# Kernel optimization log

Hardware: AMD Instinct MI355X
Metric: run time of the kernel (lower is better)

The kernel has to match this reference:

```python
import jax, jax.numpy as jnp
import numpy as np

EPS = 1e-5
N_NODES = 100000


def setup_inputs() -> dict:
    key = jax.random.key(0)
    ks = jax.random.split(key, 24)
    N, F = N_NODES, 64
    E = 1600000
    inp = {
        "x": jax.random.normal(ks[0], (N, F), dtype=jnp.float32),
        "edge_index": jax.random.randint(ks[1], (2, E), 0, N, dtype=jnp.int64),
    }
    dims = [(F, 32), (32, 64), (64, 128), (128, 1)]
    for i, (din, dout) in enumerate(dims, start=1):
        kw, kb = jax.random.split(ks[1 + i], 2)
        scale = 1.0 / np.sqrt(din)
        inp[f"W{i}"] = jax.random.uniform(kw, (din, dout), jnp.float32, -scale, scale)
        inp[f"b{i}"] = jax.random.uniform(kb, (dout,), jnp.float32, -scale, scale)
    for i, d in enumerate([32, 64, 128], start=1):
        kg, kbe, km, kv = jax.random.split(ks[8 + i], 4)
        inp[f"g{i}"] = 1.0 + 0.1 * jax.random.normal(kg, (d,), jnp.float32)
        inp[f"be{i}"] = 0.1 * jax.random.normal(kbe, (d,), jnp.float32)
        inp[f"rm{i}"] = 0.1 * jax.random.normal(km, (d,), jnp.float32)
        inp[f"rv{i}"] = 0.5 + jax.random.uniform(kv, (d,), jnp.float32)
    return inp


def _gcn_conv(x, src, dst, norm, W, b, n):
    # GCNConv: linear transform then D^-1/2 A_hat D^-1/2 aggregation (self-loops in src/dst)
    xw = x @ W  # [N, dout]
    msg = xw[src] * norm[:, None]  # [E+N, dout] gather
    return jax.ops.segment_sum(msg, dst, num_segments=n) + b


def _bn_eval(x, g, be, rm, rv):
    return (x - rm) * jax.lax.rsqrt(rv + EPS) * g + be


def reference(x, edge_index, W1, b1, W2, b2, W3, b3, W4, b4,
              g1, be1, rm1, rv1, g2, be2, rm2, rv2, g3, be3, rm3, rv3):
    n = x.shape[0]
    loop = jnp.arange(n, dtype=edge_index.dtype)
    src = jnp.concatenate([edge_index[0], loop])
    dst = jnp.concatenate([edge_index[1], loop])
    deg = jax.ops.segment_sum(jnp.ones_like(dst, dtype=x.dtype), dst, num_segments=n)
    dinv = jnp.where(deg > 0, jax.lax.rsqrt(deg), 0.0)
    norm = dinv[src] * dinv[dst]  # shared across layers

    h = _gcn_conv(x, src, dst, norm, W1, b1, n)
    h = jax.nn.elu(_bn_eval(h, g1, be1, rm1, rv1))
    h = _gcn_conv(h, src, dst, norm, W2, b2, n)
    h = jax.nn.elu(_bn_eval(h, g2, be2, rm2, rv2))
    h = _gcn_conv(h, src, dst, norm, W3, b3, n)
    h = jax.nn.elu(_bn_eval(h, g3, be3, rm3, rv3))
    h = _gcn_conv(h, src, dst, norm, W4, b4, n)
    return jax.nn.sigmoid(jax.nn.elu(h))
```

## Files before the change

kernel.cpp:

```cpp
#include <hip/hip_runtime.h>
#include <hip/hip_fp16.h>

#define EPSF 1e-5f
#define BKT_SHIFT 9
#define BKT_NODES 512
#define TILE_E 4096

__device__ __forceinline__ float elu_f(float x) { return x > 0.f ? x : expm1f(x); }

__device__ __forceinline__ float4 h4_to_f4(uint2 u) {
    __half2 a = *reinterpret_cast<const __half2*>(&u.x);
    __half2 b = *reinterpret_cast<const __half2*>(&u.y);
    float2 fa = __half22float2(a);
    float2 fb = __half22float2(b);
    return make_float4(fa.x, fa.y, fb.x, fb.y);
}
__device__ __forceinline__ uint2 f4_to_h4(float4 v) {
    __half2 a = __floats2half2_rn(v.x, v.y);
    __half2 b = __floats2half2_rn(v.z, v.w);
    uint2 u;
    u.x = *reinterpret_cast<unsigned*>(&a);
    u.y = *reinterpret_cast<unsigned*>(&b);
    return u;
}


__global__ __launch_bounds__(256) void k_zero(int* p, int n) {
    int i = blockIdx.x * 256 + threadIdx.x;
    if (i < n) p[i] = 0;
}

__global__ __launch_bounds__(256) void k_bhist(const int* __restrict__ dst, int* __restrict__ bkt_cnt, int E) {
    __shared__ int h[256];
    int t = threadIdx.x;
    h[t] = 0;
    __syncthreads();
    for (long e = (long)blockIdx.x * 256 + t; e < E; e += (long)gridDim.x * 256)
        atomicAdd(&h[dst[e] >> BKT_SHIFT], 1);
    __syncthreads();
    if (h[t]) atomicAdd(&bkt_cnt[t], h[t]);
}

__global__ __launch_bounds__(256) void k_bscan(const int* __restrict__ bkt_cnt, int* __restrict__ bbase,
                                               int* __restrict__ cursor) {
    __shared__ int sh[256];
    int t = threadIdx.x;
    int v = bkt_cnt[t];
    sh[t] = v;
    __syncthreads();
    for (int off = 1; off < 256; off <<= 1) {
        int add = (t >= off) ? sh[t - off] : 0;
        __syncthreads();
        sh[t] += add;
        __syncthreads();
    }
    int ex = sh[t] - v;
    bbase[t] = ex;
    cursor[t] = ex;
}

__global__ __launch_bounds__(256) void k_bpart(const int* __restrict__ src, const int* __restrict__ dst,
                                               int* __restrict__ cursor, int2* __restrict__ csr_tmp, int E) {
    __shared__ int hcnt[256];
    __shared__ int gbase[256];
    int t = threadIdx.x;
    long tile0 = (long)blockIdx.x * TILE_E;
    hcnt[t] = 0;
    __syncthreads();
    int d[16], s[16], rk[16];
    #pragma unroll
    for (int j = 0; j < 16; ++j) {
        long e = tile0 + j * 256 + t;
        if (e < E) {
            d[j] = dst[e];
            s[j] = src[e];
            rk[j] = atomicAdd(&hcnt[d[j] >> BKT_SHIFT], 1);
        }
    }
    __syncthreads();
    int c = hcnt[t];
    if (c) gbase[t] = atomicAdd(&cursor[t], c);
    __syncthreads();
    #pragma unroll
    for (int j = 0; j < 16; ++j) {
        long e = tile0 + j * 256 + t;
        if (e < E) {
            int2 q;
            q.x = d[j];
            q.y = s[j];
            csr_tmp[gbase[d[j] >> BKT_SHIFT] + rk[j]] = q;
        }
    }
}

__global__ __launch_bounds__(256) void k_bfine(const int2* __restrict__ csr_tmp, const int* __restrict__ bbase,
                                               const int* __restrict__ bkt_cnt, int* __restrict__ cnt,
                                               int* __restrict__ base, float* __restrict__ dinv,
                                               int* __restrict__ csr_s, int N) {
    __shared__ int cnt5[BKT_NODES];
    __shared__ int off5[BKT_NODES];
    __shared__ int sh[256];
    int b = blockIdx.x;
    int t = threadIdx.x;
    int d0 = b << BKT_SHIFT;
    int bb = bbase[b];
    int bc = bkt_cnt[b];
    cnt5[t] = 0;
    cnt5[t + 256] = 0;
    __syncthreads();
    for (int k = t; k < bc; k += 256) atomicAdd(&cnt5[csr_tmp[bb + k].x - d0], 1);
    __syncthreads();
    int v0 = cnt5[2 * t], v1 = cnt5[2 * t + 1];
    int p = v0 + v1;
    sh[t] = p;
    __syncthreads();
    for (int off = 1; off < 256; off <<= 1) {
        int add = (t >= off) ? sh[t - off] : 0;
        __syncthreads();
        sh[t] += add;
        __syncthreads();
    }
    int pre = sh[t] - p;
    off5[2 * t] = pre;
    off5[2 * t + 1] = pre + v0;
    #pragma unroll
    for (int j = 0; j < 2; ++j) {
        int idx = 2 * t + j;
        int i = d0 + idx;
        if (i < N) {
            int c = cnt5[idx];
            base[i] = bb + off5[idx];
            cnt[i] = c;
            dinv[i] = rsqrtf((float)(c + 1));
        }
    }
    __syncthreads();
    for (int k = t; k < bc; k += 256) {
        int2 e = csr_tmp[bb + k];
        int pos = bb + atomicAdd(&off5[e.x - d0], 1);
        csr_s[pos] = e.y;
    }
}

template<int F, bool L1EPI, bool HIN, bool HOUT>
__global__ __launch_bounds__(256) void k_gather(const int* __restrict__ base, const int* __restrict__ cnt,
                                                const int* __restrict__ csr_s,
                                                const float* __restrict__ dinv, const void* __restrict__ xin,
                                                const float* __restrict__ b, const float* __restrict__ g,
                                                const float* __restrict__ be, const float* __restrict__ rm,
                                                const float* __restrict__ rv, void* __restrict__ out, int n) {
    constexpr int C = F / 4;
    constexpr int NPB = 256 / C;
    int lane = threadIdx.x % C;
    int nl = threadIdx.x / C;
    int i = blockIdx.x * NPB + nl;
    if (i >= n) return;
    int k = base[i];
    int kend = k + cnt[i];
    float di = dinv[i];
    const float4* XF = reinterpret_cast<const float4*>(xin);
    const uint2*  XH = reinterpret_cast<const uint2*>(xin);
    float4 z = {0.f, 0.f, 0.f, 0.f};
    float4 a0 = z, a1 = z, a2 = z, a3 = z;
    for (; k + 3 < kend; k += 4) {
        int s0 = csr_s[k], s1 = csr_s[k + 1], s2 = csr_s[k + 2], s3 = csr_s[k + 3];
        float4 x0 = HIN ? h4_to_f4(XH[(long)s0 * C + lane]) : XF[(long)s0 * C + lane];
        float4 x1 = HIN ? h4_to_f4(XH[(long)s1 * C + lane]) : XF[(long)s1 * C + lane];
        float4 x2 = HIN ? h4_to_f4(XH[(long)s2 * C + lane]) : XF[(long)s2 * C + lane];
        float4 x3 = HIN ? h4_to_f4(XH[(long)s3 * C + lane]) : XF[(long)s3 * C + lane];
        a0.x += x0.x; a0.y += x0.y; a0.z += x0.z; a0.w += x0.w;
        a1.x += x1.x; a1.y += x1.y; a1.z += x1.z; a1.w += x1.w;
        a2.x += x2.x; a2.y += x2.y; a2.z += x2.z; a2.w += x2.w;
        a3.x += x3.x; a3.y += x3.y; a3.z += x3.z; a3.w += x3.w;
    }
    for (; k < kend; ++k) {
        int s0 = csr_s[k];
        float4 xa = HIN ? h4_to_f4(XH[(long)s0 * C + lane]) : XF[(long)s0 * C + lane];
        a0.x += xa.x; a0.y += xa.y; a0.z += xa.z; a0.w += xa.w;
    }
    float4 xs = HIN ? h4_to_f4(XH[(long)i * C + lane]) : XF[(long)i * C + lane];
    float4 o;
    o.x = di * (a0.x + a1.x + a2.x + a3.x + xs.x);
    o.y = di * (a0.y + a1.y + a2.y + a3.y + xs.y);
    o.z = di * (a0.z + a1.z + a2.z + a3.z + xs.z);
    o.w = di * (a0.w + a1.w + a2.w + a3.w + xs.w);
    if (L1EPI) {
        float4 bb = reinterpret_cast<const float4*>(b)[lane];
        float4 gg = reinterpret_cast<const float4*>(g)[lane];
        float4 ee = reinterpret_cast<const float4*>(be)[lane];
        float4 mm = reinterpret_cast<const float4*>(rm)[lane];
        float4 vv = reinterpret_cast<const float4*>(rv)[lane];
        o.x = di * elu_f((o.x + bb.x - mm.x) * rsqrtf(vv.x + EPSF) * gg.x + ee.x);
        o.y = di * elu_f((o.y + bb.y - mm.y) * rsqrtf(vv.y + EPSF) * gg.y + ee.y);
        o.z = di * elu_f((o.z + bb.z - mm.z) * rsqrtf(vv.z + EPSF) * gg.z + ee.z);
        o.w = di * elu_f((o.w + bb.w - mm.w) * rsqrtf(vv.w + EPSF) * gg.w + ee.w);
    }
    if (HOUT) reinterpret_cast<uint2*>(out)[(long)i * C + lane] = f4_to_h4(o);
    else      reinterpret_cast<float4*>(out)[(long)i * C + lane] = o;
}

__global__ __launch_bounds__(256) void k_gather1_final(const int* __restrict__ base, const int* __restrict__ cnt,
                                                       const int* __restrict__ csr_s,
                                                       const float* __restrict__ dinv, const float* __restrict__ y,
                                                       const float* __restrict__ b4, float* __restrict__ out, int n) {
    int i = blockIdx.x * 256 + threadIdx.x;
    if (i >= n) return;
    int k = base[i];
    int kend = k + cnt[i];
    float di = dinv[i];
    float acc = 0.f;
    for (; k < kend; ++k) acc += y[csr_s[k]];
    float v = di * (acc + y[i]) + b4[0];
    v = elu_f(v);
    out[i] = 1.f / (1.f + expf(-v));
}

template<int DIN, int DOUT, bool BN, bool FUSE_DOT, bool SCALE_DINV, bool HOUT>
__global__ __launch_bounds__(256, 4) void k_gemm_rt(const float* __restrict__ X, const float* __restrict__ W,
                                                    const float* __restrict__ b, const float* __restrict__ g,
                                                    const float* __restrict__ be, const float* __restrict__ rm,
                                                    const float* __restrict__ rv, const float* __restrict__ W4,
                                                    const float* __restrict__ dinv,
                                                    void* __restrict__ Y, int n) {
    constexpr int TR = 4;
    constexpr int FL = DOUT / 4;
    constexpr int RG = 256 / FL;
    constexpr int BR = RG * TR;
    __shared__ float Wl[DIN * DOUT];
    for (int idx = threadIdx.x; idx < DIN * DOUT; idx += 256) Wl[idx] = W[idx];
    __syncthreads();
    const int fl = threadIdx.x % FL;
    const int rg = threadIdx.x / FL;
    const int f0 = fl * 4;
    const long r0 = (long)blockIdx.x * BR + (long)rg * TR;

    float4 z; z.x = z.y = z.z = z.w = 0.f;
    float4 acc[TR];
    #pragma unroll
    for (int r = 0; r < TR; ++r) acc[r] = z;

    #pragma unroll 2
    for (int k0 = 0; k0 < DIN; k0 += 4) {
        float4 xv[TR];
        #pragma unroll
        for (int r = 0; r < TR; ++r) {
            long row = r0 + r;
            xv[r] = (row < n) ? *reinterpret_cast<const float4*>(X + row * DIN + k0) : z;
        }
        #pragma unroll
        for (int kk = 0; kk < 4; ++kk) {
            float4 w4 = *reinterpret_cast<const float4*>(&Wl[(k0 + kk) * DOUT + f0]);
            #pragma unroll
            for (int r = 0; r < TR; ++r) {
                float xs = (kk == 0) ? xv[r].x : (kk == 1) ? xv[r].y : (kk == 2) ? xv[r].z : xv[r].w;
                acc[r].x += xs * w4.x;
                acc[r].y += xs * w4.y;
                acc[r].z += xs * w4.z;
                acc[r].w += xs * w4.w;
            }
        }
    }

    float4 bias = z, scale = z, shift = z, w4d = z;
    if (BN) {
        bias = *reinterpret_cast<const float4*>(b + f0);
        float4 gg = *reinterpret_cast<const float4*>(g + f0);
        float4 ee = *reinterpret_cast<const float4*>(be + f0);
        float4 mm = *reinterpret_cast<const float4*>(rm + f0);
        float4 vv = *reinterpret_cast<const float4*>(rv + f0);
        scale.x = gg.x * rsqrtf(vv.x + EPSF); shift.x = ee.x - mm.x * scale.x;
        scale.y = gg.y * rsqrtf(vv.y + EPSF); shift.y = ee.y - mm.y * scale.y;
        scale.z = gg.z * rsqrtf(vv.z + EPSF); shift.z = ee.z - mm.z * scale.z;
        scale.w = gg.w * rsqrtf(vv.w + EPSF); shift.w = ee.w - mm.w * scale.w;
    }
    if (FUSE_DOT) w4d = *reinterpret_cast<const float4*>(W4 + f0);

    #pragma unroll
    for (int r = 0; r < TR; ++r) {
        long row = r0 + r;
        if (row >= n) continue;
        float4 v = acc[r];
        if (BN) {
            v.x = elu_f((v.x + bias.x) * scale.x + shift.x);
            v.y = elu_f((v.y + bias.y) * scale.y + shift.y);
            v.z = elu_f((v.z + bias.z) * scale.z + shift.z);
            v.w = elu_f((v.w + bias.w) * scale.w + shift.w);
        }
        float dv = SCALE_DINV ? dinv[row] : 1.f;
        if (FUSE_DOT) {
            float p = v.x * w4d.x + v.y * w4d.y + v.z * w4d.z + v.w * w4d.w;
            #pragma unroll
            for (int m = 1; m < FL; m <<= 1) p += __shfl_xor(p, m, 64);
            if (fl == 0) reinterpret_cast<float*>(Y)[row] = dv * p;
        } else {
            if (SCALE_DINV) { v.x *= dv; v.y *= dv; v.z *= dv; v.w *= dv; }
            if (HOUT) reinterpret_cast<uint2*>(Y)[row * FL + fl] = f4_to_h4(v);
            else      *reinterpret_cast<float4*>(reinterpret_cast<float*>(Y) + row * DOUT + f0) = v;
        }
    }
}


extern "C" void kernel_launch(void* const* d_in, const int* in_sizes, int n_in,
                              void* d_out, int out_size, void* d_ws, size_t ws_size,
                              hipStream_t stream) {
    const float* x   = (const float*)d_in[0];
    const int*   edg = (const int*)d_in[1];
    const float* W1 = (const float*)d_in[2];
    const float* b1 = (const float*)d_in[3];
    const float* W2 = (const float*)d_in[4];
    const float* b2 = (const float*)d_in[5];
    const float* W3 = (const float*)d_in[6];
    const float* b3 = (const float*)d_in[7];
    const float* W4 = (const float*)d_in[8];
    const float* b4 = (const float*)d_in[9];
    const float* g1  = (const float*)d_in[10];
    const float* be1 = (const float*)d_in[11];
    const float* rm1 = (const float*)d_in[12];
    const float* rv1 = (const float*)d_in[13];
    const float* g2  = (const float*)d_in[14];
    const float* be2 = (const float*)d_in[15];
    const float* rm2 = (const float*)d_in[16];
    const float* rv2 = (const float*)d_in[17];
    const float* g3  = (const float*)d_in[18];
    const float* be3 = (const float*)d_in[19];
    const float* rm3 = (const float*)d_in[20];
    const float* rv3 = (const float*)d_in[21];
    float* out = (float*)d_out;

    const int N = in_sizes[0] / 64;
    const int E = in_sizes[1] / 2;
    const int* src = edg;
    const int* dst = edg + E;
    const int NB_BKT = (N + BKT_NODES - 1) / BKT_NODES;
    const int NTILES = (E + TILE_E - 1) / TILE_E;

    int*   bkt_cnt = (int*)d_ws;
    int*   bbase   = bkt_cnt + 256;
    int*   cursor  = bbase + 256;
    int*   cnt     = cursor + 256;
    int*   base    = cnt + N;
    float* dinv    = (float*)(base + N);
    int*   csr_s   = (int*)(dinv + N);
    float* featA   = (float*)(csr_s + E);
    float* featB   = featA + (size_t)N * 64;
    int2*  csr_tmp = (int2*)featA;

    auto nb = [](long total) { return (int)((total + 255) / 256); };

    k_zero<<<1, 256, 0, stream>>>(bkt_cnt, 256);
    k_bhist<<<512, 256, 0, stream>>>(dst, bkt_cnt, E);
    k_bscan<<<1, 256, 0, stream>>>(bkt_cnt, bbase, cursor);
    k_bpart<<<NTILES, 256, 0, stream>>>(src, dst, cursor, csr_tmp, E);
    k_bfine<<<NB_BKT, 256, 0, stream>>>(csr_tmp, bbase, bkt_cnt, cnt, base, dinv, csr_s, N);

    k_gemm_rt<64, 32, false, false, true, true><<<(N + 127) / 128, 256, 0, stream>>>(
        x, W1, nullptr, nullptr, nullptr, nullptr, nullptr, nullptr, dinv, featB, N);
    k_gather<32, true, true, true><<<(N + 31) / 32, 256, 0, stream>>>(base, cnt, csr_s, dinv, featB,
                                                                      b1, g1, be1, rm1, rv1, featA, N);

    k_gather<32, false, true, false><<<(N + 31) / 32, 256, 0, stream>>>(base, cnt, csr_s, dinv, featA,
                                                                        nullptr, nullptr, nullptr, nullptr, nullptr,
                                                                        featB, N);
    k_gemm_rt<32, 64, true, false, true, true><<<(N + 63) / 64, 256, 0, stream>>>(
        featB, W2, b2, g2, be2, rm2, rv2, nullptr, dinv, featA, N);

    k_gather<64, false, true, false><<<(N + 15) / 16, 256, 0, stream>>>(base, cnt, csr_s, dinv, featA,
                                                                        nullptr, nullptr, nullptr, nullptr, nullptr,
                                                                        featB, N);
    k_gemm_rt<64, 128, true, true, true, false><<<(N + 31) / 32, 256, 0, stream>>>(
        featB, W3, b3, g3, be3, rm3, rv3, W4, dinv, featA, N);

    k_gather1_final<<<nb(N), 256, 0, stream>>>(base, cnt, csr_s, dinv, featA, b4, out, N);
}
```

Before: 366.0 us.

## Fuse aggregation with dense transform for layers 2 and 3 using fp16 dot2

Replaces the separate gather and GEMM kernels for layers 2 and 3 with single kernels. Each kernel aggregates neighbor features into shared memory, then multiplies by an fp16-packed weight tile using the fdot2 instruction, followed by BN, ELU and dinv scaling. This removes the intermediate global write and read of the aggregated features. In exchange, every block reconverts the weights to half in shared memory, and the matmul now runs in fp16 with fp32 accumulation, which adds precision risk.

New measurement: 343.9 us. -6.1%, faster.

```diff
diff --git a/kernel.cpp b/kernel.cpp
--- a/kernel.cpp
+++ b/kernel.cpp
@@ -6,7 +6,18 @@
 #define BKT_NODES 512
 #define TILE_E 4096
 
+typedef _Float16 half2_t __attribute__((ext_vector_type(2)));
+
 __device__ __forceinline__ float elu_f(float x) { return x > 0.f ? x : expm1f(x); }
+
+__device__ __forceinline__ float fdot2f(half2_t a, half2_t b, float c) {
+#if __has_builtin(__builtin_amdgcn_fdot2)
+    return __builtin_amdgcn_fdot2(a, b, c, false);
+#else
+    return c + (float)a.x * (float)b.x + (float)a.y * (float)b.y;
+#endif
+}
+__device__ __forceinline__ half2_t bch2(unsigned u) { return __builtin_bit_cast(half2_t, u); }
 
 __device__ __forceinline__ float4 h4_to_f4(uint2 u) {
     __half2 a = *reinterpret_cast<const __half2*>(&u.x);
@@ -300,6 +311,212 @@
     }
 }
 
+__global__ __launch_bounds__(256, 4) void k_fuse2(const int* __restrict__ base, const int* __restrict__ cnt,
+                                                  const int* __restrict__ csr_s, const float* __restrict__ dinv,
+                                                  const uint2* __restrict__ Xh,
+                                                  const float* __restrict__ W, const float* __restrict__ b,
+                                                  const float* __restrict__ g, const float* __restrict__ be,
+                                                  const float* __restrict__ rm, const float* __restrict__ rv,
+                                                  uint2* __restrict__ Y,
+                                                  int n) {
+    __shared__ half2_t Wl2[16 * 64];
+    __shared__ __align__(16) uint2 T2[32 * 8];
+    __shared__ float Dl[32];
+    int t = threadIdx.x;
+    for (int idx = t; idx < 16 * 64; idx += 256) {
+        int p = idx >> 6, j = idx & 63;
+        half2_t w;
+        w.x = (_Float16)W[(2 * p) * 64 + j];
+        w.y = (_Float16)W[(2 * p + 1) * 64 + j];
+        Wl2[idx] = w;
+    }
+    int lane = t & 7, nl = t >> 3;
+    long i = (long)blockIdx.x * 32 + nl;
+    float4 z = {0.f, 0.f, 0.f, 0.f};
+    float4 o = z;
+    float di = 0.f;
+    if (i < n) {
+        int k = base[i], kend = k + cnt[i];
+        di = dinv[i];
+        float4 a0 = z, a1 = z;
+        for (; k + 1 < kend; k += 2) {
+            int s0 = csr_s[k], s1 = csr_s[k + 1];
+            float4 x0 = h4_to_f4(Xh[(long)s0 * 8 + lane]);
+            float4 x1 = h4_to_f4(Xh[(long)s1 * 8 + lane]);
+            a0.x += x0.x; a0.y += x0.y; a0.z += x0.z; a0.w += x0.w;
+            a1.x += x1.x; a1.y += x1.y; a1.z += x1.z; a1.w += x1.w;
+        }
+        if (k < kend) {
+            float4 xa = h4_to_f4(Xh[(long)csr_s[k] * 8 + lane]);
+            a0.x += xa.x; a0.y += xa.y; a0.z += xa.z; a0.w += xa.w;
+        }
+        float4 xs = h4_to_f4(Xh[(long)i * 8 + lane]);
+        o.x = di * (a0.x + a1.x + xs.x);
+        o.y = di * (a0.y + a1.y + xs.y);
+        o.z = di * (a0.z + a1.z + xs.z);
+        o.w = di * (a0.w + a1.w + xs.w);
+    }
+    T2[nl * 8 + lane] = f4_to_h4(o);
+    if (lane == 0) Dl[nl] = di;
+    __syncthreads();
+
+    int fl = t & 15, rg = t >> 4;
+    int f0 = fl * 4;
+    const uint4* T4 = reinterpret_cast<const uint4*>(T2);
+    float4 acc0 = z, acc1 = z;
+    #pragma unroll
+    for (int c = 0; c < 4; ++c) {
+        uint4 ra = T4[(rg * 2 + 0) * 4 + c];
+        uint4 rb = T4[(rg * 2 + 1) * 4 + c];
+        #pragma unroll
+        for (int q = 0; q < 4; ++q) {
+            uint4 wv = *reinterpret_cast<const uint4*>(&Wl2[(c * 4 + q) * 64 + f0]);
+            half2_t w0 = bch2(wv.x), w1 = bch2(wv.y), w2 = bch2(wv.z), w3 = bch2(wv.w);
+            unsigned ua = (q == 0) ? ra.x : (q == 1) ? ra.y : (q == 2) ? ra.z : ra.w;
+            unsigned ub = (q == 0) ? rb.x : (q == 1) ? rb.y : (q == 2) ? rb.z : rb.w;
+            half2_t xa = bch2(ua), xb = bch2(ub);
+            acc0.x = fdot2f(xa, w0, acc0.x); acc0.y = fdot2f(xa, w1, acc0.y);
+            acc0.z = fdot2f(xa, w2, acc0.z); acc0.w = fdot2f(xa, w3, acc0.w);
+            acc1.x = fdot2f(xb, w0, acc1.x); acc1.y = fdot2f(xb, w1, acc1.y);
+            acc1.z = fdot2f(xb, w2, acc1.z); acc1.w = fdot2f(xb, w3, acc1.w);
+        }
+    }
+    float4 bias = *reinterpret_cast<const float4*>(b + f0);
+    float4 gg = *reinterpret_cast<const float4*>(g + f0);
+    float4 ee = *reinterpret_cast<const float4*>(be + f0);
+    float4 mm = *reinterpret_cast<const float4*>(rm + f0);
+    float4 vv = *reinterpret_cast<const float4*>(rv + f0);
+    float4 scale, shift;
+    scale.x = gg.x * rsqrtf(vv.x + EPSF); shift.x = ee.x - mm.x * scale.x;
+    scale.y = gg.y * rsqrtf(vv.y + EPSF); shift.y = ee.y - mm.y * scale.y;
+    scale.z = gg.z * rsqrtf(vv.z + EPSF); shift.z = ee.z - mm.z * scale.z;
+    scale.w = gg.w * rsqrtf(vv.w + EPSF); shift.w = ee.w - mm.w * scale.w;
+    #pragma unroll
+    for (int r = 0; r < 2; ++r) {
+        long row = (long)blockIdx.x * 32 + rg * 2 + r;
+        if (row >= n) continue;
+        float4 v = r ? acc1 : acc0;
+        float dv = Dl[rg * 2 + r];
+        v.x = dv * elu_f((v.x + bias.x) * scale.x + shift.x);
+        v.y = dv * elu_f((v.y + bias.y) * scale.y + shift.y);
+        v.z = dv * elu_f((v.z + bias.z) * scale.z + shift.z);
+        v.w = dv * elu_f((v.w + bias.w) * scale.w + shift.w);
+        Y[row * 16 + fl] = f4_to_h4(v);
+    }
+}
+
+__global__ __launch_bounds__(256, 4) void k_fuse3(const int* __restrict__ base, const int* __restrict__ cnt,
+                                                  const int* __restrict__ csr_s, const float* __restrict__ dinv,
+                                                  const uint4* __restrict__ Xh,
+                                                  const float* __restrict__ W, const float* __restrict__ b,
+                                                  const float* __restrict__ g, const float* __restrict__ be,
+                                                  const float* __restrict__ rm, const float* __restrict__ rv,
+                                                  const float* __restrict__ W4,
+                                                  float* __restrict__ y, int n) {
+    __shared__ half2_t Wl2[32 * 128];
+    __shared__ uint4 T3[32 * 8];
+    __shared__ float Dl[32];
+    int t = threadIdx.x;
+    for (int idx = t; idx < 32 * 128; idx += 256) {
+        int p = idx >> 7, j = idx & 127;
+        half2_t w;
+        w.x = (_Float16)W[(2 * p) * 128 + j];
+        w.y = (_Float16)W[(2 * p + 1) * 128 + j];
+        Wl2[idx] = w;
+    }
+    int lane = t & 7, nl = t >> 3;
+    long i = (long)blockIdx.x * 32 + nl;
+    float4 z = {0.f, 0.f, 0.f, 0.f};
+    float4 oLo = z, oHi = z;
+    float di = 0.f;
+    if (i < n) {
+        int k = base[i], kend = k + cnt[i];
+        di = dinv[i];
+        float4 aL0 = z, aH0 = z, aL1 = z, aH1 = z;
+        for (; k + 1 < kend; k += 2) {
+            int s0 = csr_s[k], s1 = csr_s[k + 1];
+            uint4 u0 = Xh[(long)s0 * 8 + lane];
+            uint4 u1 = Xh[(long)s1 * 8 + lane];
+            float4 l0 = h4_to_f4(make_uint2(u0.x, u0.y)), h0 = h4_to_f4(make_uint2(u0.z, u0.w));
+            float4 l1 = h4_to_f4(make_uint2(u1.x, u1.y)), h1 = h4_to_f4(make_uint2(u1.z, u1.w));
+            aL0.x += l0.x; aL0.y += l0.y; aL0.z += l0.z; aL0.w += l0.w;
+            aH0.x += h0.x; aH0.y += h0.y; aH0.z += h0.z; aH0.w += h0.w;
+            aL1.x += l1.x; aL1.y += l1.y; aL1.z += l1.z; aL1.w += l1.w;
+            aH1.x += h1.x; aH1.y += h1.y; aH1.z += h1.z; aH1.w += h1.w;
+        }
+        if (k < kend) {
+            uint4 u0 = Xh[(long)csr_s[k] * 8 + lane];
+            float4 l0 = h4_to_f4(make_uint2(u0.x, u0.y)), h0 = h4_to_f4(make_uint2(u0.z, u0.w));
+            aL0.x += l0.x; aL0.y += l0.y; aL0.z += l0.z; aL0.w += l0.w;
+            aH0.x += h0.x; aH0.y += h0.y; aH0.z += h0.z; aH0.w += h0.w;
+        }
+        uint4 us = Xh[(long)i * 8 + lane];
+        float4 ls = h4_to_f4(make_uint2(us.x, us.y)), hs = h4_to_f4(make_uint2(us.z, us.w));
+        oLo.x = di * (aL0.x + aL1.x + ls.x);
+        oLo.y = di * (aL0.y + aL1.y + ls.y);
+        oLo.z = di * (aL0.z + aL1.z + ls.z);
+        oLo.w = di * (aL0.w + aL1.w + ls.w);
+        oHi.x = di * (aH0.x + aH1.x + hs.x);
+        oHi.y = di * (aH0.y + aH1.y + hs.y);
+        oHi.z = di * (aH0.z + aH1.z + hs.z);
+        oHi.w = di * (aH0.w + aH1.w + hs.w);
+    }
+    uint2 pl = f4_to_h4(oLo), ph = f4_to_h4(oHi);
+    uint4 packed; packed.x = pl.x; packed.y = pl.y; packed.z = ph.x; packed.w = ph.y;
+    T3[nl * 8 + lane] = packed;
+    if (lane == 0) Dl[nl] = di;
+    __syncthreads();
+
+    int fl = t & 31, rg = t >> 5;
+    int f0 = fl * 4;
+    float4 acc[4] = {z, z, z, z};
+    #pragma unroll 2
+    for (int c = 0; c < 8; ++c) {
+        uint4 rowc[4];
+        #pragma unroll
+        for (int r = 0; r < 4; ++r) rowc[r] = T3[(rg * 4 + r) * 8 + c];
+        #pragma unroll
+        for (int q = 0; q < 4; ++q) {
+            uint4 wv = *reinterpret_cast<const uint4*>(&Wl2[(c * 4 + q) * 128 + f0]);
+            half2_t w0 = bch2(wv.x), w1 = bch2(wv.y), w2 = bch2(wv.z), w3 = bch2(wv.w);
+            #pragma unroll
+            for (int r = 0; r < 4; ++r) {
+                unsigned xu = (q == 0) ? rowc[r].x : (q == 1) ? rowc[r].y : (q == 2) ? rowc[r].z : rowc[r].w;
+                half2_t xp = bch2(xu);
+                acc[r].x = fdot2f(xp, w0, acc[r].x);
+                acc[r].y = fdot2f(xp, w1, acc[r].y);
+                acc[r].z = fdot2f(xp, w2, acc[r].z);
+                acc[r].w = fdot2f(xp, w3, acc[r].w);
+            }
+        }
+    }
+    float4 bias = *reinterpret_cast<const float4*>(b + f0);
+    float4 gg = *reinterpret_cast<const float4*>(g + f0);
+    float4 ee = *reinterpret_cast<const float4*>(be + f0);
+    float4 mm = *reinterpret_cast<const float4*>(rm + f0);
+    float4 vv = *reinterpret_cast<const float4*>(rv + f0);
+    float4 w4d = *reinterpret_cast<const float4*>(W4 + f0);
+    float4 scale, shift;
+    scale.x = gg.x * rsqrtf(vv.x + EPSF); shift.x = ee.x - mm.x * scale.x;
+    scale.y = gg.y * rsqrtf(vv.y + EPSF); shift.y = ee.y - mm.y * scale.y;
+    scale.z = gg.z * rsqrtf(vv.z + EPSF); shift.z = ee.z - mm.z * scale.z;
+    scale.w = gg.w * rsqrtf(vv.w + EPSF); shift.w = ee.w - mm.w * scale.w;
+    #pragma unroll
+    for (int r = 0; r < 4; ++r) {
+        long row = (long)blockIdx.x * 32 + rg * 4 + r;
+        if (row >= n) continue;
+        float4 v = acc[r];
+        v.x = elu_f((v.x + bias.x) * scale.x + shift.x);
+        v.y = elu_f((v.y + bias.y) * scale.y + shift.y);
+        v.z = elu_f((v.z + bias.z) * scale.z + shift.z);
+        v.w = elu_f((v.w + bias.w) * scale.w + shift.w);
+        float p = v.x * w4d.x + v.y * w4d.y + v.z * w4d.z + v.w * w4d.w;
+        #pragma unroll
+        for (int m = 1; m < 32; m <<= 1) p += __shfl_xor(p, m, 64);
+        if (fl == 0) y[row] = Dl[rg * 4 + r] * p;
+    }
+}
+
 
 extern "C" void kernel_launch(void* const* d_in, const int* in_sizes, int n_in,
                               void* d_out, int out_size, void* d_ws, size_t ws_size,
@@ -359,17 +576,11 @@
     k_gather<32, true, true, true><<<(N + 31) / 32, 256, 0, stream>>>(base, cnt, csr_s, dinv, featB,
                                                                       b1, g1, be1, rm1, rv1, featA, N);
 
-    k_gather<32, false, true, false><<<(N + 31) / 32, 256, 0, stream>>>(base, cnt, csr_s, dinv, featA,
-                                                                        nullptr, nullptr, nullptr, nullptr, nullptr,
-                                                                        featB, N);
-    k_gemm_rt<32, 64, true, false, true, true><<<(N + 63) / 64, 256, 0, stream>>>(
-        featB, W2, b2, g2, be2, rm2, rv2, nullptr, dinv, featA, N);
-
-    k_gather<64, false, true, false><<<(N + 15) / 16, 256, 0, stream>>>(base, cnt, csr_s, dinv, featA,
-                                                                        nullptr, nullptr, nullptr, nullptr, nullptr,
-                                                                        featB, N);
-    k_gemm_rt<64, 128, true, true, true, false><<<(N + 31) / 32, 256, 0, stream>>>(
-        featB, W3, b3, g3, be3, rm3, rv3, W4, dinv, featA, N);
+    k_fuse2<<<(N + 31) / 32, 256, 0, stream>>>(base, cnt, csr_s, dinv, (const uint2*)featA,
+                                               W2, b2, g2, be2, rm2, rv2, (uint2*)featB, N);
+
+    k_fuse3<<<(N + 31) / 32, 256, 0, stream>>>(base, cnt, csr_s, dinv, (const uint4*)featB,
+                                               W3, b3, g3, be3, rm3, rv3, W4, featA, N);
 
     k_gather1_final<<<nb(N), 256, 0, stream>>>(base, cnt, csr_s, dinv, featA, b4, out, N);
 }
```
